# Kernel optimization log

Hardware: AMD Instinct MI355X
Metric: run time of the kernel (lower is better)

## Reference

```python
import jax, jax.numpy as jnp
import numpy as np
from jax import lax

D = 1024          # d_model
ORDER = 2         # hyena order
FILT = 64         # filter_order (implicit MLP width)
EMB = 3           # positional embedding dim (default)
INNER = D * (ORDER + 1)
DF = D * (ORDER - 1)   # filter d_model
L_MAX = 2048


def setup_inputs() -> dict:
    key = jax.random.key(0)
    ks = jax.random.split(key, 16)
    s = 0.02
    return {
        "u": jax.random.normal(ks[0], (4, L_MAX, D), jnp.float32),
        "in_w": jax.random.normal(ks[1], (D, INNER), jnp.float32) * s,
        "in_b": jnp.zeros((INNER,), jnp.float32),
        "short_w": jax.random.normal(ks[2], (INNER, 3), jnp.float32) * 0.3,
        "short_b": jnp.zeros((INNER,), jnp.float32),
        "mlp_w1": jax.random.normal(ks[3], (EMB, FILT), jnp.float32) * 0.3,
        "mlp_b1": jnp.zeros((FILT,), jnp.float32),
        "mlp_w2": jax.random.normal(ks[4], (FILT, FILT), jnp.float32) * 0.1,
        "mlp_b2": jnp.zeros((FILT,), jnp.float32),
        "mlp_w3": jax.random.normal(ks[5], (FILT, FILT), jnp.float32) * 0.1,
        "mlp_b3": jnp.zeros((FILT,), jnp.float32),
        "mlp_wo": jax.random.normal(ks[6], (FILT, DF), jnp.float32) * 0.1,
        "freq": jnp.ones((1, FILT), jnp.float32),       # shared Sin freq (w=1)
        "filt_bias": jax.random.normal(ks[7], (DF,), jnp.float32),
        "out_w": jax.random.normal(ks[8], (D, D), jnp.float32) * s,
        "out_b": jnp.zeros((D,), jnp.float32),
    }


def _pos_emb(L):
    # PositionalEmbedding(emb_dim=3): t, real/imag of exp(-i f w), bands=(3-1)//2=1
    t = jnp.linspace(0.0, 1.0, L)[:, None]                      # (L,1)
    tr = jnp.linspace(0.0, L - 1.0, L)[:, None]
    w = 2.0 * np.pi * tr / L                                    # (L,1)
    f = jnp.array([1e-4], jnp.float32)[None, :]                  # bands=1
    z = jnp.concatenate([t, jnp.cos(f * w), -jnp.sin(f * w)], axis=-1)  # (L,3)
    return z, t


def _decay(t):
    # ExponentialModulation: target=1e-2, fast=0.3, slow=1.5, shift=0
    max_d = np.log(1e-2) / 0.3
    min_d = np.log(1e-2) / 1.5
    deltas = jnp.linspace(min_d, max_d, DF)[None, :]             # (1,DF)
    return jnp.exp(-t * jnp.abs(deltas))                         # (L,DF)


def reference(u, in_w, in_b, short_w, short_b, mlp_w1, mlp_b1, mlp_w2, mlp_b2,
              mlp_w3, mlp_b3, mlp_wo, freq, filt_bias, out_w, out_b):
    B, L, _ = u.shape
    # in_proj: b l d -> b l (3d) -> b (3d) l
    up = jnp.einsum('bld,de->ble', u, in_w) + in_b
    up = up.transpose(0, 2, 1)                                   # (B, INNER, L)
    # depthwise short conv, kernel 3, padding 2 both sides, then [:L]
    uc = lax.conv_general_dilated(up, short_w[:, None, :], (1,), [(2, 2)],
                                  feature_group_count=INNER,
                                  dimension_numbers=('NCH', 'OIH', 'NCH'))
    uc = uc[..., :L] + short_b[None, :, None]
    x0, x1, v = uc[:, :D], uc[:, D:2 * D], uc[:, 2 * D:]
    # implicit long filter k(L): pos-emb -> Sin MLP (shared freq) -> modulation
    z, t = _pos_emb(L)
    h = jnp.sin(freq * (z @ mlp_w1 + mlp_b1))
    h = jnp.sin(freq * (h @ mlp_w2 + mlp_b2))
    h = jnp.sin(freq * (h @ mlp_w3 + mlp_b3))
    h = h @ mlp_wo                                               # (L, DF)
    k = (h * _decay(t)).T                                        # (DF, L) == (D, L) for order=2
    # hyena recurrence: order-1 = 1 gated fft-conv step
    vx = v * x1                                                  # (B, D, L)
    n = 2 * L
    y = jnp.fft.irfft(jnp.fft.rfft(vx, n=n) * jnp.fft.rfft(k, n=n), n=n)[..., :L]
    v = y + vx * filt_bias[None, :, None]
    # final gate + out_proj
    yv = (v * x0).transpose(0, 2, 1)                             # (B, L, D)
    return jnp.einsum('bld,de->ble', yv, out_w) + out_b
```

## Files before the change

### kernel.cpp

```cpp
#include <hip/hip_runtime.h>
#include <math.h>

#define M_PIf 3.14159265358979323846f
#define MIND (-3.0701134573253936f)
#define MAXD (-15.350567286626968f)

typedef __attribute__((ext_vector_type(8))) _Float16 f16x8;
typedef __attribute__((ext_vector_type(4))) float f32x4;

#define GLDS(g, l) __builtin_amdgcn_global_load_lds(                         \
    (const __attribute__((address_space(1))) void*)(g),                      \
    (__attribute__((address_space(3))) void*)(l), 16, 0, 0)

__device__ __forceinline__ unsigned short f2h(float x) {
    return __builtin_bit_cast(unsigned short, (_Float16)x);
}
__device__ __forceinline__ float h2f(unsigned short h) {
    return (float)__builtin_bit_cast(_Float16, h);
}

__global__ __launch_bounds__(256) void split_kernel(
    const float* __restrict__ in, unsigned short* __restrict__ out, int n4)
{
    int i = blockIdx.x * 256 + threadIdx.x;
    if (i >= n4) return;
    float4 v = ((const float4*)in)[i];
    ushort4 h;
    h.x = f2h(v.x); h.y = f2h(v.y); h.z = f2h(v.z); h.w = f2h(v.w);
    ((ushort4*)out)[i] = h;
}

__global__ __launch_bounds__(256) void tsplit_kernel(
    const float* __restrict__ in, unsigned short* __restrict__ out,
    int R, int C, long in_zstride, long out_zstride)
{
    __shared__ float t[32][33];
    const float* inz = in + (size_t)blockIdx.z * in_zstride;
    const int r0 = blockIdx.y * 32, c0 = blockIdx.x * 32;
    const int tx = threadIdx.x & 31, ty = threadIdx.x >> 5;
#pragma unroll
    for (int q = 0; q < 4; ++q) {
        int r = ty + q * 8;
        t[r][tx] = inz[(size_t)(r0 + r) * C + c0 + tx];
    }
    __syncthreads();
#pragma unroll
    for (int q = 0; q < 4; ++q) {
        int cc = ty + q * 8;
        size_t o = (size_t)blockIdx.z * out_zstride + (size_t)(c0 + cc) * R + r0 + tx;
        out[o] = f2h(t[tx][cc]);
    }
}

template <int TRANS_OUT>
__global__ __launch_bounds__(256, 2) void gemm_f16_kernel(
    const unsigned short* __restrict__ A, const unsigned short* __restrict__ B,
    const float* __restrict__ bias, float* __restrict__ outp)
{
    __shared__ char smem[36864];
    const int tid = threadIdx.x;
    const int wave = tid >> 6, lane = tid & 63;
    const int n0 = blockIdx.x * 128, m0 = blockIdx.y * 128;
    const int wm = wave >> 1, wn = wave & 1;

    f32x4 acc[4][4] = {};

    const int srow = lane >> 2;
    const int scol = (lane & 3) * 16;

    auto stage = [&](int buf, int t) {
        const int k0 = t * 32;
        char* base = smem + buf * 16384;
#pragma unroll
        for (int ld = 0; ld < 2; ++ld) {
            const int rchunk = wave * 32 + ld * 16;
            const int r = rchunk + srow;
            GLDS((const char*)(A + (size_t)(m0 + r) * 1024 + k0) + scol,
                 base + 0 * 8192 + rchunk * 64);
            GLDS((const char*)(B + (size_t)(n0 + r) * 1024 + k0) + scol,
                 base + 1 * 8192 + rchunk * 64);
        }
    };

    stage(0, 0);
    asm volatile("s_waitcnt vmcnt(0)");
    __syncthreads();
    int cur = 0;
    const int rr = lane & 15, gg = (lane >> 4) * 16;
    for (int t = 0; t < 32; ++t) {
        if (t < 31) stage(cur ^ 1, t + 1);
        const char* b = smem + cur * 16384;
        f16x8 ah[4], bh[4];
#pragma unroll
        for (int i = 0; i < 4; ++i) {
            ah[i] = *(const f16x8*)(b + 0 * 8192 + (wm * 64 + i * 16 + rr) * 64 + gg);
            bh[i] = *(const f16x8*)(b + 1 * 8192 + (wn * 64 + i * 16 + rr) * 64 + gg);
        }
#pragma unroll
        for (int i = 0; i < 4; ++i)
#pragma unroll
            for (int j = 0; j < 4; ++j)
                acc[i][j] = __builtin_amdgcn_mfma_f32_16x16x32_f16(ah[i], bh[j], acc[i][j], 0, 0, 0);
        __syncthreads();
        cur ^= 1;
    }

    const int c = lane & 15, g4 = lane >> 4;
    if (TRANS_OUT) {
        float* scr = (float*)smem + wave * (32 * 68);
        const int bidx = m0 >> 11;
        const int lbase = (m0 & 2047) + wm * 64;
#pragma unroll
        for (int p = 0; p < 2; ++p) {
#pragma unroll
            for (int j = 0; j < 2; ++j) {
                const int jj = p * 2 + j;
                const float bv = bias[n0 + wn * 64 + jj * 16 + c];
#pragma unroll
                for (int i = 0; i < 4; ++i)
#pragma unroll
                    for (int r = 0; r < 4; ++r)
                        scr[(j * 16 + c) * 68 + i * 16 + g4 * 4 + r] = acc[i][jj][r] + bv;
            }
#pragma unroll
            for (int it = 0; it < 8; ++it) {
                const int row = it * 4 + g4;
                float4 v = *(const float4*)&scr[row * 68 + c * 4];
                const int e = n0 + wn * 64 + p * 32 + row;
                *(float4*)&outp[((size_t)bidx * 3072 + e) * 2048 + lbase + c * 4] = v;
            }
            __syncthreads();
        }
    } else {
#pragma unroll
        for (int j = 0; j < 4; ++j) {
            const int col = n0 + wn * 64 + j * 16 + c;
            const float bv = bias[col];
#pragma unroll
            for (int i = 0; i < 4; ++i) {
                const int row = m0 + wm * 64 + i * 16 + g4 * 4;
#pragma unroll
                for (int r = 0; r < 4; ++r)
                    outp[(size_t)(row + r) * 1024 + col] = acc[i][j][r] + bv;
            }
        }
    }
}

__global__ __launch_bounds__(256) void filt_kernel(
    const float* __restrict__ w1, const float* __restrict__ b1,
    const float* __restrict__ w2, const float* __restrict__ b2,
    const float* __restrict__ w3, const float* __restrict__ b3,
    const float* __restrict__ wo, const float* __restrict__ freq,
    float* __restrict__ kbuf)
{
    __shared__ float ha[8][65], hb[8][65];
    const int l0 = blockIdx.x * 8;
    const int tid = threadIdx.x;
    const int uu = tid & 63, lq = tid >> 6;
#pragma unroll
    for (int p = 0; p < 2; ++p) {
        int ll = lq + p * 4;
        int l = l0 + ll;
        float t = (float)l * (1.0f / 2047.0f);
        float ang = 1e-4f * (2.0f * M_PIf) * ((float)l / 2048.0f);
        float pre = t * w1[uu] + cosf(ang) * w1[64 + uu] - sinf(ang) * w1[128 + uu] + b1[uu];
        ha[ll][uu] = sinf(freq[uu] * pre);
    }
    __syncthreads();
#pragma unroll
    for (int p = 0; p < 2; ++p) {
        int ll = lq + p * 4;
        float s = b2[uu];
#pragma unroll
        for (int i = 0; i < 64; ++i) s += ha[ll][i] * w2[i * 64 + uu];
        hb[ll][uu] = sinf(freq[uu] * s);
    }
    __syncthreads();
#pragma unroll
    for (int p = 0; p < 2; ++p) {
        int ll = lq + p * 4;
        float s = b3[uu];
#pragma unroll
        for (int i = 0; i < 64; ++i) s += hb[ll][i] * w3[i * 64 + uu];
        ha[ll][uu] = sinf(freq[uu] * s);
    }
    __syncthreads();

    float acc[4][8] = {};
    for (int i = 0; i < 64; ++i) {
        float wv[4];
#pragma unroll
        for (int q = 0; q < 4; ++q) wv[q] = wo[i * 1024 + tid + 256 * q];
#pragma unroll
        for (int l = 0; l < 8; ++l) {
            float hv = ha[l][i];
#pragma unroll
            for (int q = 0; q < 4; ++q) acc[q][l] += hv * wv[q];
        }
    }
    const float span = (MAXD - MIND) * (1.0f / 1023.0f);
#pragma unroll
    for (int q = 0; q < 4; ++q) {
        int dd = tid + 256 * q;
        float ad = fabsf(MIND + span * (float)dd);
#pragma unroll
        for (int l = 0; l < 8; ++l) {
            float t = (float)(l0 + l) * (1.0f / 2047.0f);
            kbuf[(size_t)dd * 2048 + l0 + l] = acc[q][l] * expf(-t * ad);
        }
    }
}

__global__ __launch_bounds__(256, 2) void conv_kernel(
    const float* __restrict__ up_t, const float* __restrict__ kbuf,
    const float* __restrict__ sw, const float* __restrict__ sb,
    const float* __restrict__ fbias, float* __restrict__ yv)
{
    __shared__ char smem[35840];
#define VH(b) ((unsigned short*)(smem + (b) * 4608))
    int* wpk = (int*)(smem + 18432);
    float* x0p = (float*)(smem + 18432);

    const int d = blockIdx.x;
    const int tid = threadIdx.x;

    const float* kr = kbuf + (size_t)d * 2048;
    for (int x = tid; x < 2064; x += 256) {
        int k1 = 2047 - x;
        float f1 = (k1 >= 0) ? kr[k1] : 0.f;
        float f2 = (k1 >= 1) ? kr[k1 - 1] : 0.f;
        wpk[x] = (int)((unsigned)f2h(f1) | ((unsigned)f2h(f2) << 16));
    }
    const float w1a = sw[(1024 + d) * 3 + 0], w1b = sw[(1024 + d) * 3 + 1], w1c = sw[(1024 + d) * 3 + 2];
    const float w2a = sw[(2048 + d) * 3 + 0], w2b = sw[(2048 + d) * 3 + 1], w2c = sw[(2048 + d) * 3 + 2];
    const float sb1 = sb[1024 + d], sb2 = sb[2048 + d];
    for (int idx = tid; idx < 2304; idx += 256) {
        int l = idx - 240;
#pragma unroll
        for (int b = 0; b < 4; ++b) {
            float vx = 0.f;
            if (l >= 0 && l < 2048) {
                const float* rx1 = up_t + ((size_t)(b * 3072) + 1024 + d) * 2048;
                const float* rv  = up_t + ((size_t)(b * 3072) + 2048 + d) * 2048;
                float a2 = (l >= 2) ? rx1[l - 2] : 0.f;
                float a1 = (l >= 1) ? rx1[l - 1] : 0.f;
                float x1 = w1a * a2 + w1b * a1 + w1c * rx1[l] + sb1;
                float c2 = (l >= 2) ? rv[l - 2] : 0.f;
                float c1 = (l >= 1) ? rv[l - 1] : 0.f;
                float vv = w2a * c2 + w2b * c1 + w2c * rv[l] + sb2;
                vx = vv * x1;
            }
            VH(b)[idx] = f2h(vx);
        }
    }
    __syncthreads();

    const int wv = tid >> 6, lane = tid & 63;
    const int row = lane & 15;
    const int sseg = lane >> 4;
    f32x4 acc[2][4] = {};
#pragma unroll
    for (int gi = 0; gi < 2; ++gi) {
        const int g = gi ? (7 - wv) : wv;
        const int tmax = 8 * g + 8;
        int xA = 2031 - row + 8 * sseg;
        int xB = 224 + 256 * g + 16 * row + 8 * sseg;
        for (int t = 0; t < tmax; ++t) {
            int4 avh;
            avh.x = wpk[xA];     avh.y = wpk[xA + 2];
            avh.z = wpk[xA + 4]; avh.w = wpk[xA + 6];
            f16x8 ah = __builtin_bit_cast(f16x8, avh);
#pragma unroll
            for (int b = 0; b < 4; ++b) {
                f16x8 bh = *(const f16x8*)(VH(b) + xB);
                acc[gi][b] = __builtin_amdgcn_mfma_f32_16x16x32_f16(ah, bh, acc[gi][b], 0, 0, 0);
            }
            xA -= 32;
            xB -= 32;
        }
    }

    const float w0a = sw[d * 3 + 0], w0b = sw[d * 3 + 1], w0c = sw[d * 3 + 2];
    const float sb0 = sb[d];
    const float fb = fbias[d];
#pragma unroll
    for (int half = 0; half < 2; ++half) {
        __syncthreads();
        for (int l = tid; l < 2048; l += 256) {
#pragma unroll
            for (int bb = 0; bb < 2; ++bb) {
                const int b = half * 2 + bb;
                const float* r0 = up_t + ((size_t)(b * 3072) + d) * 2048;
                float a2 = (l >= 2) ? r0[l - 2] : 0.f;
                float a1 = (l >= 1) ? r0[l - 1] : 0.f;
                x0p[bb * 2176 + l + (l >> 4)] = w0a * a2 + w0b * a1 + w0c * r0[l] + sb0;
            }
        }
        __syncthreads();
#pragma unroll
        for (int gi = 0; gi < 2; ++gi) {
            const int g = gi ? (7 - wv) : wv;
            const int lb = 256 * g + 16 * row + 4 * sseg;
#pragma unroll
            for (int bb = 0; bb < 2; ++bb) {
                const int b = half * 2 + bb;
                ushort4 vhq = *(const ushort4*)(VH(b) + 240 + lb);
                const float* xp = x0p + bb * 2176;
                const int xi = lb + (lb >> 4);
                f32x4 a = acc[gi][b];
                float4 o;
                o.x = (a[0] + h2f(vhq.x) * fb) * xp[xi + 0];
                o.y = (a[1] + h2f(vhq.y) * fb) * xp[xi + 1];
                o.z = (a[2] + h2f(vhq.z) * fb) * xp[xi + 2];
                o.w = (a[3] + h2f(vhq.w) * fb) * xp[xi + 3];
                *(float4*)&yv[((size_t)(b * 1024) + d) * 2048 + lb] = o;
            }
        }
    }
#undef VH
}

extern "C" void kernel_launch(void* const* d_in, const int* in_sizes, int n_in,
                              void* d_out, int out_size, void* d_ws, size_t ws_size,
                              hipStream_t stream) {
    (void)in_sizes; (void)n_in; (void)out_size; (void)ws_size;
    const float* u         = (const float*)d_in[0];
    const float* in_w      = (const float*)d_in[1];
    const float* in_b      = (const float*)d_in[2];
    const float* short_w   = (const float*)d_in[3];
    const float* short_b   = (const float*)d_in[4];
    const float* mlp_w1    = (const float*)d_in[5];
    const float* mlp_b1    = (const float*)d_in[6];
    const float* mlp_w2    = (const float*)d_in[7];
    const float* mlp_b2    = (const float*)d_in[8];
    const float* mlp_w3    = (const float*)d_in[9];
    const float* mlp_b3    = (const float*)d_in[10];
    const float* mlp_wo    = (const float*)d_in[11];
    const float* freq      = (const float*)d_in[12];
    const float* filt_bias = (const float*)d_in[13];
    const float* out_w     = (const float*)d_in[14];
    const float* out_b     = (const float*)d_in[15];
    float* out = (float*)d_out;

    char* ws = (char*)d_ws;
    const size_t MB = 1024 * 1024;
    float*          up_t  = (float*)ws;
    unsigned short* yvt   = (unsigned short*)ws;
    float*          kbuf  = (float*)(ws + 96 * MB);
    unsigned short* uh    = (unsigned short*)(ws + 104 * MB);
    unsigned short* w1t   = (unsigned short*)(ws + 120 * MB);
    float*          yvb   = (float*)(ws + 104 * MB);
    unsigned short* w2t   = (unsigned short*)(ws + 136 * MB);

    hipLaunchKernelGGL(split_kernel, dim3(8192), dim3(256), 0, stream,
                       u, uh, 8192 * 1024 / 4);
    hipLaunchKernelGGL(tsplit_kernel, dim3(96, 32, 1), dim3(256), 0, stream,
                       in_w, w1t, 1024, 3072, 0L, 0L);
    hipLaunchKernelGGL(filt_kernel, dim3(256), dim3(256), 0, stream,
                       mlp_w1, mlp_b1, mlp_w2, mlp_b2, mlp_w3, mlp_b3, mlp_wo, freq, kbuf);
    hipLaunchKernelGGL((gemm_f16_kernel<1>), dim3(24, 64), dim3(256), 0, stream,
                       uh, w1t, in_b, up_t);
    hipLaunchKernelGGL(conv_kernel, dim3(1024), dim3(256), 0, stream,
                       up_t, kbuf, short_w, short_b, filt_bias, yvb);
    hipLaunchKernelGGL(tsplit_kernel, dim3(64, 32, 4), dim3(256), 0, stream,
                       yvb, yvt, 1024, 2048, 1024L * 2048L, 2048L * 1024L);
    hipLaunchKernelGGL(tsplit_kernel, dim3(32, 32, 1), dim3(256), 0, stream,
                       out_w, w2t, 1024, 1024, 0L, 0L);
    hipLaunchKernelGGL((gemm_f16_kernel<0>), dim3(8, 64), dim3(256), 0, stream,
                       yvt, w2t, out_b, out);
}
```

Before: 205.9 us.

## Store intermediate activations in fp16 to halve memory traffic between stages

The in-projection GEMM now writes its transposed output directly as fp16 with 4-wide stores, dropping the fp32 LDS staging path. The conv kernel reads fp16 inputs, computes the x0 gate for all four batches up front into a larger LDS region, and writes fp16 output. A new fp16-to-fp16 transpose kernel replaces the fp32 transpose-and-convert step before the out-projection. This targets the large fp32 intermediate buffers. The cost is extra rounding of activations, more LDS per conv block, and uncoalesced 8-byte strided stores from the GEMM epilogue.

```diff
diff --git a/kernel.cpp b/kernel.cpp
--- a/kernel.cpp
+++ b/kernel.cpp
@@ -32,32 +32,54 @@
 
 __global__ __launch_bounds__(256) void tsplit_kernel(
     const float* __restrict__ in, unsigned short* __restrict__ out,
-    int R, int C, long in_zstride, long out_zstride)
+    int R, int C)
 {
     __shared__ float t[32][33];
-    const float* inz = in + (size_t)blockIdx.z * in_zstride;
     const int r0 = blockIdx.y * 32, c0 = blockIdx.x * 32;
     const int tx = threadIdx.x & 31, ty = threadIdx.x >> 5;
 #pragma unroll
     for (int q = 0; q < 4; ++q) {
         int r = ty + q * 8;
-        t[r][tx] = inz[(size_t)(r0 + r) * C + c0 + tx];
+        t[r][tx] = in[(size_t)(r0 + r) * C + c0 + tx];
     }
     __syncthreads();
 #pragma unroll
     for (int q = 0; q < 4; ++q) {
         int cc = ty + q * 8;
-        size_t o = (size_t)blockIdx.z * out_zstride + (size_t)(c0 + cc) * R + r0 + tx;
-        out[o] = f2h(t[tx][cc]);
+        out[(size_t)(c0 + cc) * R + r0 + tx] = f2h(t[tx][cc]);
+    }
+}
+
+__global__ __launch_bounds__(256) void t16_kernel(
+    const unsigned short* __restrict__ in, unsigned short* __restrict__ out)
+{
+    __shared__ unsigned short t[64][66];
+    const int b = blockIdx.z;
+    const int d0 = blockIdx.y * 64, l0 = blockIdx.x * 64;
+    const int tid = threadIdx.x;
+    const int rr = tid >> 4, cc = (tid & 15) * 4;
+#pragma unroll
+    for (int p = 0; p < 4; ++p) {
+        int r = p * 16 + rr;
+        ushort4 v = *(const ushort4*)&in[((size_t)b * 1024 + d0 + r) * 2048 + l0 + cc];
+        t[cc + 0][r] = v.x; t[cc + 1][r] = v.y; t[cc + 2][r] = v.z; t[cc + 3][r] = v.w;
+    }
+    __syncthreads();
+#pragma unroll
+    for (int p = 0; p < 4; ++p) {
+        int r = p * 16 + rr;
+        ushort4 o;
+        o.x = t[r][cc + 0]; o.y = t[r][cc + 1]; o.z = t[r][cc + 2]; o.w = t[r][cc + 3];
+        *(ushort4*)&out[((size_t)b * 2048 + l0 + r) * 1024 + d0 + cc] = o;
     }
 }
 
 template <int TRANS_OUT>
 __global__ __launch_bounds__(256, 2) void gemm_f16_kernel(
     const unsigned short* __restrict__ A, const unsigned short* __restrict__ B,
-    const float* __restrict__ bias, float* __restrict__ outp)
-{
-    __shared__ char smem[36864];
+    const float* __restrict__ bias, void* __restrict__ outp)
+{
+    __shared__ char smem[32768];
     const int tid = threadIdx.x;
     const int wave = tid >> 6, lane = tid & 63;
     const int n0 = blockIdx.x * 128, m0 = blockIdx.y * 128;
@@ -107,31 +129,26 @@
 
     const int c = lane & 15, g4 = lane >> 4;
     if (TRANS_OUT) {
-        float* scr = (float*)smem + wave * (32 * 68);
+        unsigned short* up = (unsigned short*)outp;
         const int bidx = m0 >> 11;
-        const int lbase = (m0 & 2047) + wm * 64;
-#pragma unroll
-        for (int p = 0; p < 2; ++p) {
-#pragma unroll
-            for (int j = 0; j < 2; ++j) {
-                const int jj = p * 2 + j;
-                const float bv = bias[n0 + wn * 64 + jj * 16 + c];
-#pragma unroll
-                for (int i = 0; i < 4; ++i)
-#pragma unroll
-                    for (int r = 0; r < 4; ++r)
-                        scr[(j * 16 + c) * 68 + i * 16 + g4 * 4 + r] = acc[i][jj][r] + bv;
+        const int lbase = (m0 & 2047) + wm * 64 + g4 * 4;
+#pragma unroll
+        for (int j = 0; j < 4; ++j) {
+            const int e = n0 + wn * 64 + j * 16 + c;
+            const float bv = bias[e];
+            unsigned short* dst = up + ((size_t)bidx * 3072 + e) * 2048 + lbase;
+#pragma unroll
+            for (int i = 0; i < 4; ++i) {
+                ushort4 o;
+                o.x = f2h(acc[i][j][0] + bv);
+                o.y = f2h(acc[i][j][1] + bv);
+                o.z = f2h(acc[i][j][2] + bv);
+                o.w = f2h(acc[i][j][3] + bv);
+                *(ushort4*)(dst + i * 16) = o;
             }
-#pragma unroll
-            for (int it = 0; it < 8; ++it) {
-                const int row = it * 4 + g4;
-                float4 v = *(const float4*)&scr[row * 68 + c * 4];
-                const int e = n0 + wn * 64 + p * 32 + row;
-                *(float4*)&outp[((size_t)bidx * 3072 + e) * 2048 + lbase + c * 4] = v;
-            }
-            __syncthreads();
         }
     } else {
+        float* op = (float*)outp;
 #pragma unroll
         for (int j = 0; j < 4; ++j) {
             const int col = n0 + wn * 64 + j * 16 + c;
@@ -141,7 +158,7 @@
                 const int row = m0 + wm * 64 + i * 16 + g4 * 4;
 #pragma unroll
                 for (int r = 0; r < 4; ++r)
-                    outp[(size_t)(row + r) * 1024 + col] = acc[i][j][r] + bv;
+                    op[(size_t)(row + r) * 1024 + col] = acc[i][j][r] + bv;
             }
         }
     }
@@ -213,14 +230,14 @@
 }
 
 __global__ __launch_bounds__(256, 2) void conv_kernel(
-    const float* __restrict__ up_t, const float* __restrict__ kbuf,
+    const unsigned short* __restrict__ up_t, const float* __restrict__ kbuf,
     const float* __restrict__ sw, const float* __restrict__ sb,
-    const float* __restrict__ fbias, float* __restrict__ yv)
-{
-    __shared__ char smem[35840];
+    const float* __restrict__ fbias, unsigned short* __restrict__ yv)
+{
+    __shared__ char smem[47168];
 #define VH(b) ((unsigned short*)(smem + (b) * 4608))
+#define X0(b) ((unsigned short*)(smem + 26688 + (b) * 5120))
     int* wpk = (int*)(smem + 18432);
-    float* x0p = (float*)(smem + 18432);
 
     const int d = blockIdx.x;
     const int tid = threadIdx.x;
@@ -234,24 +251,34 @@
     }
     const float w1a = sw[(1024 + d) * 3 + 0], w1b = sw[(1024 + d) * 3 + 1], w1c = sw[(1024 + d) * 3 + 2];
     const float w2a = sw[(2048 + d) * 3 + 0], w2b = sw[(2048 + d) * 3 + 1], w2c = sw[(2048 + d) * 3 + 2];
-    const float sb1 = sb[1024 + d], sb2 = sb[2048 + d];
+    const float w0a = sw[d * 3 + 0], w0b = sw[d * 3 + 1], w0c = sw[d * 3 + 2];
+    const float sb1 = sb[1024 + d], sb2 = sb[2048 + d], sb0 = sb[d];
     for (int idx = tid; idx < 2304; idx += 256) {
         int l = idx - 240;
 #pragma unroll
         for (int b = 0; b < 4; ++b) {
             float vx = 0.f;
             if (l >= 0 && l < 2048) {
-                const float* rx1 = up_t + ((size_t)(b * 3072) + 1024 + d) * 2048;
-                const float* rv  = up_t + ((size_t)(b * 3072) + 2048 + d) * 2048;
-                float a2 = (l >= 2) ? rx1[l - 2] : 0.f;
-                float a1 = (l >= 1) ? rx1[l - 1] : 0.f;
-                float x1 = w1a * a2 + w1b * a1 + w1c * rx1[l] + sb1;
-                float c2 = (l >= 2) ? rv[l - 2] : 0.f;
-                float c1 = (l >= 1) ? rv[l - 1] : 0.f;
-                float vv = w2a * c2 + w2b * c1 + w2c * rv[l] + sb2;
+                const unsigned short* rx1 = up_t + ((size_t)(b * 3072) + 1024 + d) * 2048;
+                const unsigned short* rv  = up_t + ((size_t)(b * 3072) + 2048 + d) * 2048;
+                float a2 = (l >= 2) ? h2f(rx1[l - 2]) : 0.f;
+                float a1 = (l >= 1) ? h2f(rx1[l - 1]) : 0.f;
+                float x1 = w1a * a2 + w1b * a1 + w1c * h2f(rx1[l]) + sb1;
+                float c2 = (l >= 2) ? h2f(rv[l - 2]) : 0.f;
+                float c1 = (l >= 1) ? h2f(rv[l - 1]) : 0.f;
+                float vv = w2a * c2 + w2b * c1 + w2c * h2f(rv[l]) + sb2;
                 vx = vv * x1;
             }
             VH(b)[idx] = f2h(vx);
+        }
+    }
+    for (int l = tid; l < 2048; l += 256) {
+#pragma unroll
+        for (int b = 0; b < 4; ++b) {
+            const unsigned short* r0 = up_t + ((size_t)(b * 3072) + d) * 2048;
+            float a2 = (l >= 2) ? h2f(r0[l - 2]) : 0.f;
+            float a1 = (l >= 1) ? h2f(r0[l - 1]) : 0.f;
+            X0(b)[l + 4 * (l >> 4)] = f2h(w0a * a2 + w0b * a1 + w0c * h2f(r0[l]) + sb0);
         }
     }
     __syncthreads();
@@ -281,44 +308,26 @@
         }
     }
 
-    const float w0a = sw[d * 3 + 0], w0b = sw[d * 3 + 1], w0c = sw[d * 3 + 2];
-    const float sb0 = sb[d];
     const float fb = fbias[d];
 #pragma unroll
-    for (int half = 0; half < 2; ++half) {
-        __syncthreads();
-        for (int l = tid; l < 2048; l += 256) {
-#pragma unroll
-            for (int bb = 0; bb < 2; ++bb) {
-                const int b = half * 2 + bb;
-                const float* r0 = up_t + ((size_t)(b * 3072) + d) * 2048;
-                float a2 = (l >= 2) ? r0[l - 2] : 0.f;
-                float a1 = (l >= 1) ? r0[l - 1] : 0.f;
-                x0p[bb * 2176 + l + (l >> 4)] = w0a * a2 + w0b * a1 + w0c * r0[l] + sb0;
-            }
-        }
-        __syncthreads();
-#pragma unroll
-        for (int gi = 0; gi < 2; ++gi) {
-            const int g = gi ? (7 - wv) : wv;
-            const int lb = 256 * g + 16 * row + 4 * sseg;
-#pragma unroll
-            for (int bb = 0; bb < 2; ++bb) {
-                const int b = half * 2 + bb;
-                ushort4 vhq = *(const ushort4*)(VH(b) + 240 + lb);
-                const float* xp = x0p + bb * 2176;
-                const int xi = lb + (lb >> 4);
-                f32x4 a = acc[gi][b];
-                float4 o;
-                o.x = (a[0] + h2f(vhq.x) * fb) * xp[xi + 0];
-                o.y = (a[1] + h2f(vhq.y) * fb) * xp[xi + 1];
-                o.z = (a[2] + h2f(vhq.z) * fb) * xp[xi + 2];
-                o.w = (a[3] + h2f(vhq.w) * fb) * xp[xi + 3];
-                *(float4*)&yv[((size_t)(b * 1024) + d) * 2048 + lb] = o;
-            }
+    for (int gi = 0; gi < 2; ++gi) {
+        const int g = gi ? (7 - wv) : wv;
+        const int lb = 256 * g + 16 * row + 4 * sseg;
+#pragma unroll
+        for (int b = 0; b < 4; ++b) {
+            ushort4 vhq = *(const ushort4*)(VH(b) + 240 + lb);
+            ushort4 x0q = *(const ushort4*)(X0(b) + lb + 4 * (lb >> 4));
+            f32x4 a = acc[gi][b];
+            ushort4 o;
+            o.x = f2h((a[0] + h2f(vhq.x) * fb) * h2f(x0q.x));
+            o.y = f2h((a[1] + h2f(vhq.y) * fb) * h2f(x0q.y));
+            o.z = f2h((a[2] + h2f(vhq.z) * fb) * h2f(x0q.z));
+            o.w = f2h((a[3] + h2f(vhq.w) * fb) * h2f(x0q.w));
+            *(ushort4*)&yv[((size_t)(b * 1024) + d) * 2048 + lb] = o;
         }
     }
 #undef VH
+#undef X0
 }
 
 extern "C" void kernel_launch(void* const* d_in, const int* in_sizes, int n_in,
@@ -345,28 +354,28 @@
 
     char* ws = (char*)d_ws;
     const size_t MB = 1024 * 1024;
-    float*          up_t  = (float*)ws;
-    unsigned short* yvt   = (unsigned short*)ws;
-    float*          kbuf  = (float*)(ws + 96 * MB);
-    unsigned short* uh    = (unsigned short*)(ws + 104 * MB);
-    unsigned short* w1t   = (unsigned short*)(ws + 120 * MB);
-    float*          yvb   = (float*)(ws + 104 * MB);
-    unsigned short* w2t   = (unsigned short*)(ws + 136 * MB);
+    unsigned short* up_t = (unsigned short*)ws;
+    unsigned short* yvh  = (unsigned short*)(ws + 48 * MB);
+    unsigned short* yvt  = (unsigned short*)(ws + 64 * MB);
+    unsigned short* w2t  = (unsigned short*)(ws + 80 * MB);
+    float*          kbuf = (float*)(ws + 82 * MB);
+    unsigned short* uh   = (unsigned short*)(ws + 90 * MB);
+    unsigned short* w1t  = (unsigned short*)(ws + 106 * MB);
 
     hipLaunchKernelGGL(split_kernel, dim3(8192), dim3(256), 0, stream,
                        u, uh, 8192 * 1024 / 4);
-    hipLaunchKernelGGL(tsplit_kernel, dim3(96, 32, 1), dim3(256), 0, stream,
-                       in_w, w1t, 1024, 3072, 0L, 0L);
+    hipLaunchKernelGGL(tsplit_kernel, dim3(96, 32), dim3(256), 0, stream,
+                       in_w, w1t, 1024, 3072);
     hipLaunchKernelGGL(filt_kernel, dim3(256), dim3(256), 0, stream,
                        mlp_w1, mlp_b1, mlp_w2, mlp_b2, mlp_w3, mlp_b3, mlp_wo, freq, kbuf);
     hipLaunchKernelGGL((gemm_f16_kernel<1>), dim3(24, 64), dim3(256), 0, stream,
-                       uh, w1t, in_b, up_t);
+                       uh, w1t, in_b, (void*)up_t);
     hipLaunchKernelGGL(conv_kernel, dim3(1024), dim3(256), 0, stream,
-                       up_t, kbuf, short_w, short_b, filt_bias, yvb);
-    hipLaunchKernelGGL(tsplit_kernel, dim3(64, 32, 4), dim3(256), 0, stream,
-                       yvb, yvt, 1024, 2048, 1024L * 2048L, 2048L * 1024L);
-    hipLaunchKernelGGL(tsplit_kernel, dim3(32, 32, 1), dim3(256), 0, stream,
-                       out_w, w2t, 1024, 1024, 0L, 0L);
+                       up_t, kbuf, short_w, short_b, filt_bias, yvh);
+    hipLaunchKernelGGL(t16_kernel, dim3(32, 16, 4), dim3(256), 0, stream,
+                       yvh, yvt);
+    hipLaunchKernelGGL(tsplit_kernel, dim3(32, 32), dim3(256), 0, stream,
+                       out_w, w2t, 1024, 1024);
     hipLaunchKernelGGL((gemm_f16_kernel<0>), dim3(8, 64), dim3(256), 0, stream,
-                       yvt, w2t, out_b, out);
-}
+                       yvt, w2t, out_b, (void*)out);
+}
```

Measured after the change: 282.0 us. +37.0%, slower.
